# Performance work log

Measured on AMD Instinct MI355X. Metric: run time of the kernel, lower is better.

## Reference

```python
import jax, jax.numpy as jnp
from jax import lax
import numpy as np
import math

B, S, I, H = 64, 512, 1024, 1024


def setup_inputs() -> dict:
    key = jax.random.key(0)
    kx, kw, ku, kb = jax.random.split(key, 4)
    stdv = 1.0 / math.sqrt(H)
    x = jax.random.normal(kx, (B, S, I), dtype=jnp.float32)
    # fused gate weights, order [i, f, g, o] along last axis
    W = jax.random.uniform(kw, (I, 4 * H), minval=-stdv, maxval=stdv, dtype=jnp.float32)
    U = jax.random.uniform(ku, (H, 4 * H), minval=-stdv, maxval=stdv, dtype=jnp.float32)
    b = jax.random.uniform(kb, (4 * H,), minval=-stdv, maxval=stdv, dtype=jnp.float32)
    return {"x": x, "W": W, "U": U, "b": b}


def reference(x, W, U, b):
    bsz, seq, _ = x.shape
    hid = U.shape[0]
    # precompute input projection for all timesteps: one big GEMM
    xW = jnp.einsum("bsi,ig->bsg", x, W) + b  # [B, S, 4H]

    def step(carry, xw_t):
        h, c = carry
        gates = xw_t + h @ U  # [B, 4H]
        i_t, f_t, g_t, o_t = jnp.split(gates, 4, axis=-1)
        i_t = jax.nn.sigmoid(i_t)
        f_t = jax.nn.sigmoid(f_t)
        g_t = jnp.tanh(g_t)
        o_t = jax.nn.sigmoid(o_t)
        c = f_t * c + i_t * g_t
        h = o_t * jnp.tanh(c)
        return (h, c), h

    h0 = jnp.zeros((bsz, hid), dtype=x.dtype)
    c0 = jnp.zeros((bsz, hid), dtype=x.dtype)
    (h_t, c_t), hs = lax.scan(step, (h0, c0), xW.transpose(1, 0, 2))
    hidden_seq = hs.transpose(1, 0, 2)  # [B, S, H]
    return hidden_seq, h_t, c_t
```

## Files before the change

kernel.cpp:

```cpp
#include <hip/hip_runtime.h>

#define BB 64
#define SS 512
#define II 1024
#define HH 1024
#define G4 4096
#define NWG_REC 64

typedef unsigned short u16;
typedef unsigned int u32;
typedef unsigned long long u64;

typedef short s16x8 __attribute__((ext_vector_type(8)));
typedef float f32x4 __attribute__((ext_vector_type(4)));

typedef __attribute__((address_space(1))) const u32 as1_uint_t;
typedef __attribute__((address_space(3))) u32 as3_uint_t;

__device__ __forceinline__ u16 f2bf(float f) {
    u32 x = __float_as_uint(f);
    x += 0x7fffu + ((x >> 16) & 1u);
    return (u16)(x >> 16);
}
__device__ __forceinline__ float bf2f(u16 v) {
    return __uint_as_float(((u32)v) << 16);
}
__device__ __forceinline__ f32x4 mfma16(s16x8 a, s16x8 b, f32x4 c) {
    return __builtin_amdgcn_mfma_f32_16x16x32_bf16(a, b, c, 0, 0, 0);
}
__device__ __forceinline__ float fsigm(float x) { return 1.f / (1.f + __expf(-x)); }
__device__ __forceinline__ float ftanh(float x) {
    float e = __expf(2.f * x);
    return (e - 1.f) / (e + 1.f);
}

#define HL(dst, ptr, OFF) \
    asm volatile("global_load_dwordx4 %0, %1, off offset:%2 sc0 sc1" \
                 : "=v"(dst) : "v"(ptr), "n"(OFF))
#define XL32(dst, ptr) \
    asm volatile("global_load_dword %0, %1, off" : "=v"(dst) : "v"(ptr))
#define XL16(dst, ptr) \
    asm volatile("global_load_ushort %0, %1, off" : "=v"(dst) : "v"(ptr))
#define WAITAV(N, A) \
    asm volatile("s_waitcnt vmcnt(%8)" \
                 : "+v"((A)[0]), "+v"((A)[1]), "+v"((A)[2]), "+v"((A)[3]), \
                   "+v"((A)[4]), "+v"((A)[5]), "+v"((A)[6]), "+v"((A)[7]) \
                 : "n"(N))

__global__ __launch_bounds__(256) void k_convert_x(const float* __restrict__ x,
                                                   u16* __restrict__ xb, int n4) {
    int i = blockIdx.x * 256 + threadIdx.x;
    int stride = gridDim.x * 256;
    const float4* xv = (const float4*)x;
    u64* ov = (u64*)xb;
    for (; i < n4; i += stride) {
        float4 v = xv[i];
        u64 o = (u64)f2bf(v.x) | ((u64)f2bf(v.y) << 16) |
                ((u64)f2bf(v.z) << 32) | ((u64)f2bf(v.w) << 48);
        ov[i] = o;
    }
}

__global__ __launch_bounds__(1024) void k_transpose_bf(const float* __restrict__ A,
                                                       u16* __restrict__ At, int R, int C) {
    __shared__ float tile[32][33];
    int cb = blockIdx.x * 32, rb = blockIdx.y * 32;
    int tx = threadIdx.x, ty = threadIdx.y;
    tile[ty][tx] = A[(size_t)(rb + ty) * C + cb + tx];
    __syncthreads();
    At[(size_t)(cb + ty) * R + rb + tx] = f2bf(tile[tx][ty]);
}

__global__ __launch_bounds__(256) void k_zero(u64* hb, u32* cnt) {
    int i = blockIdx.x * 256 + threadIdx.x;
    int stride = gridDim.x * 256;
    const int n = 2 * BB * HH * 2 / 8;
    for (; i < n; i += stride) hb[i] = 0ull;
    if (blockIdx.x == 0 && threadIdx.x == 0) *cnt = 0u;
}

template <bool XW32>
__global__ __launch_bounds__(256) void k_gemm_xw(const u16* __restrict__ Abf,
                                                 const u16* __restrict__ Bt,
                                                 const float* __restrict__ bias,
                                                 void* __restrict__ xw) {
    __shared__ u16 As[128 * 32];
    __shared__ u16 Bs[128 * 32];
    int bid = blockIdx.x;
    int wid = (bid & 7) * 1024 + (bid >> 3);
    int mt = wid & 255, nt = wid >> 8;
    size_t rb = (size_t)mt * 128;
    int cb = nt * 128;
    int tid = threadIdx.x;
    int w = tid >> 6, l = tid & 63;
    int lr = l >> 4, lc = l & 15;
    int wr = (w >> 1) * 64, wc = (w & 1) * 64;
    f32x4 acc[4][4] = {};
    for (int kb = 0; kb < II; kb += 32) {
        __syncthreads();
#pragma unroll
        for (int q = 0; q < 2; ++q) {
            int bo = q * 4096 + w * 1024 + l * 16;
            int row = bo >> 6;
            int off = (bo & 63) >> 1;
            const u16* srcA = Abf + (rb + row) * II + kb + off;
            __builtin_amdgcn_global_load_lds((as1_uint_t*)srcA,
                (as3_uint_t*)((char*)As + q * 4096 + w * 1024), 16, 0, 0);
            const u16* srcB = Bt + (size_t)(cb + row) * II + kb + off;
            __builtin_amdgcn_global_load_lds((as1_uint_t*)srcB,
                (as3_uint_t*)((char*)Bs + q * 4096 + w * 1024), 16, 0, 0);
        }
        __syncthreads();
        s16x8 af[4], bf[4];
#pragma unroll
        for (int m = 0; m < 4; ++m)
            af[m] = *(const s16x8*)(As + (wr + m * 16 + lc) * 32 + lr * 8);
#pragma unroll
        for (int n = 0; n < 4; ++n)
            bf[n] = *(const s16x8*)(Bs + (wc + n * 16 + lc) * 32 + lr * 8);
#pragma unroll
        for (int m = 0; m < 4; ++m)
#pragma unroll
            for (int n = 0; n < 4; ++n)
                acc[m][n] = mfma16(af[m], bf[n], acc[m][n]);
    }
    float bv[4];
#pragma unroll
    for (int n = 0; n < 4; ++n) bv[n] = bias[cb + wc + n * 16 + lc];
#pragma unroll
    for (int m = 0; m < 4; ++m) {
#pragma unroll
        for (int r = 0; r < 4; ++r) {
            size_t g = rb + wr + m * 16 + lr * 4 + r;
            size_t srow = ((g & 511) << 6) | (g >> 9);
#pragma unroll
            for (int n = 0; n < 4; ++n) {
                float v = acc[m][n][r] + bv[n];
                size_t idx = srow * G4 + cb + wc + n * 16 + lc;
                if (XW32) ((float*)xw)[idx] = v;
                else      ((u16*)xw)[idx] = f2bf(v);
            }
        }
    }
}

template <bool XW32>
__global__ __launch_bounds__(256, 1) void k_lstm3(const u16* __restrict__ Ut,
                                                  const void* __restrict__ xw,
                                                  u16* hb, u32* cnt,
                                                  float* __restrict__ out) {
    __shared__ u16 Us[8192 * 8];
    const int j = blockIdx.x;
    const int tid = threadIdx.x;
    const int w = tid >> 6, l = tid & 63;
    const int lr = l >> 4, lc = l & 15;
    const int rowbase = w * 16;
    const int col = j * 16 + lc;

    for (int i = 0; i < 32; ++i) {
        int ch = tid + (i << 8);
        int lc2 = ch & 15, lr2 = (ch >> 4) & 3, g2 = (ch >> 6) & 3, kk2 = ch >> 8;
        const u16* src = Ut + (size_t)(g2 * HH + j * 16 + lc2) * II + kk2 * 32 + lr2 * 8;
        *(s16x8*)(Us + (size_t)ch * 8) = *(const s16x8*)src;
    }

    float cc[4] = {0.f, 0.f, 0.f, 0.f};
    const size_t xwlane = (size_t)(rowbase + lr * 4) * G4 + col;

    const char* xwp[16];
#pragma unroll
    for (int g = 0; g < 4; ++g)
#pragma unroll
        for (int r = 0; r < 4; ++r) {
            size_t e = (size_t)BB * G4 + xwlane + (size_t)r * G4 + (size_t)g * HH;
            xwp[g * 4 + r] = (const char*)xw + (XW32 ? e * 4 : e * 2);
        }

    float cur[16];
#pragma unroll
    for (int g = 0; g < 4; ++g)
#pragma unroll
        for (int r = 0; r < 4; ++r) {
            size_t e = xwlane + (size_t)r * G4 + (size_t)g * HH;
            cur[g * 4 + r] = XW32 ? ((const float*)xw)[e] : bf2f(((const u16*)xw)[e]);
        }
    __syncthreads();

    for (int t = 0; t < SS; ++t) {
        f32x4 acc[4][4];
#pragma unroll
        for (int g = 0; g < 4; ++g) {
#pragma unroll
            for (int r = 0; r < 4; ++r) acc[g][0][r] = cur[g * 4 + r];
            acc[g][1] = f32x4{0.f, 0.f, 0.f, 0.f};
            acc[g][2] = f32x4{0.f, 0.f, 0.f, 0.f};
            acc[g][3] = f32x4{0.f, 0.f, 0.f, 0.f};
        }

        const u16* hrow = hb + (size_t)(t & 1) * (BB * HH) +
                          (size_t)(rowbase + lc) * HH + lr * 8;
        s16x8 av[32];
#pragma unroll
        for (int kk = 0; kk < 32; ++kk) HL(av[kk], hrow, kk * 64);

        u32 nxt[16];
#pragma unroll
        for (int q = 0; q < 16; ++q) {
            if (XW32) { XL32(nxt[q], xwp[q]); }
            else      { XL16(nxt[q], xwp[q]); }
        }

#pragma unroll
        for (int kb = 0; kb < 4; ++kb) {
            WAITAV(40 - 8 * kb, av + kb * 8);
#pragma unroll
            for (int u = 0; u < 8; ++u) {
                const int kk = kb * 8 + u;
#pragma unroll
                for (int g = 0; g < 4; ++g) {
                    const s16x8 bv = *(const s16x8*)(Us + (size_t)(((kk * 4 + g) * 4 + lr) * 16 + lc) * 8);
                    acc[g][kk & 3] = mfma16(av[kk], bv, acc[g][kk & 3]);
                }
            }
        }

        u16* hwr = hb + (size_t)((t + 1) & 1) * (BB * HH);
        float hval[4];
#pragma unroll
        for (int r = 0; r < 4; ++r) {
            float gi = (acc[0][0][r] + acc[0][1][r]) + (acc[0][2][r] + acc[0][3][r]);
            float gf = (acc[1][0][r] + acc[1][1][r]) + (acc[1][2][r] + acc[1][3][r]);
            float gg = (acc[2][0][r] + acc[2][1][r]) + (acc[2][2][r] + acc[2][3][r]);
            float go = (acc[3][0][r] + acc[3][1][r]) + (acc[3][2][r] + acc[3][3][r]);
            float i_ = fsigm(gi);
            float f_ = fsigm(gf);
            float g_ = ftanh(gg);
            float o_ = fsigm(go);
            cc[r] = f_ * cc[r] + i_ * g_;
            hval[r] = o_ * ftanh(cc[r]);
        }
#pragma unroll
        for (int r = 0; r < 4; ++r) {
            int row = rowbase + lr * 4 + r;
            out[(size_t)row * (SS * HH) + (size_t)t * HH + col] = hval[r];
            if (t < SS - 1) {
                __hip_atomic_store(hwr + (size_t)row * HH + col, f2bf(hval[r]),
                                   __ATOMIC_RELAXED, __HIP_MEMORY_SCOPE_AGENT);
            } else {
                out[(size_t)(BB * SS * HH) + (size_t)row * HH + col] = hval[r];
                out[(size_t)(BB * SS * HH + BB * HH) + (size_t)row * HH + col] = cc[r];
            }
        }

        if (t < SS - 1) {
            asm volatile("s_waitcnt vmcnt(0)"
                         : "+v"(nxt[0]), "+v"(nxt[1]), "+v"(nxt[2]), "+v"(nxt[3]),
                           "+v"(nxt[4]), "+v"(nxt[5]), "+v"(nxt[6]), "+v"(nxt[7]),
                           "+v"(nxt[8]), "+v"(nxt[9]), "+v"(nxt[10]), "+v"(nxt[11]),
                           "+v"(nxt[12]), "+v"(nxt[13]), "+v"(nxt[14]), "+v"(nxt[15]));
            __syncthreads();
            if (tid == 0) {
                u32 target = (u32)(t + 1) * NWG_REC;
                u32 old = __hip_atomic_fetch_add(cnt, 1u, __ATOMIC_RELAXED,
                                                 __HIP_MEMORY_SCOPE_AGENT);
                if (old != target - 1) {
                    while (__hip_atomic_load(cnt, __ATOMIC_RELAXED,
                                             __HIP_MEMORY_SCOPE_AGENT) < target)
                        __builtin_amdgcn_s_sleep(1);
                }
            }
            __syncthreads();
            if (t < SS - 2) {
#pragma unroll
                for (int q = 0; q < 16; ++q)
                    xwp[q] += (size_t)BB * G4 * (XW32 ? 4 : 2);
            }
        }
#pragma unroll
        for (int q = 0; q < 16; ++q)
            cur[q] = XW32 ? __uint_as_float(nxt[q]) : __uint_as_float(nxt[q] << 16);
    }
}

extern "C" void kernel_launch(void* const* d_in, const int* in_sizes, int n_in,
                              void* d_out, int out_size, void* d_ws, size_t ws_size,
                              hipStream_t stream) {
    const float* x = (const float*)d_in[0];
    const float* W = (const float*)d_in[1];
    const float* U = (const float*)d_in[2];
    const float* b = (const float*)d_in[3];
    float* out = (float*)d_out;

    size_t xb_b  = (size_t)BB * SS * II * 2;
    size_t wt_b  = (size_t)G4 * II * 2;
    size_t hb_b  = (size_t)2 * BB * HH * 2;
    size_t xw32_b = (size_t)BB * SS * G4 * 4;
    size_t xw16_b = xw32_b / 2;
    size_t base = xb_b + 2 * wt_b;

    int mode = (base + xw32_b + hb_b + 256 <= ws_size) ? 0 : 1;

    char* p = (char*)d_ws;
    u16* xb = (u16*)p;
    u16* Wt = (u16*)(p + xb_b);
    u16* Ut = (u16*)(p + xb_b + wt_b);
    char* q = p + base;
    void* xw = (void*)q;
    q += (mode == 0) ? xw32_b : xw16_b;
    u16* hb = (u16*)q; q += hb_b;
    u32* cnt = (u32*)q;

    k_convert_x<<<2048, 256, 0, stream>>>(x, xb, BB * SS * II / 4);
    k_transpose_bf<<<dim3(G4 / 32, II / 32), dim3(32, 32), 0, stream>>>(W, Wt, II, G4);
    k_transpose_bf<<<dim3(G4 / 32, II / 32), dim3(32, 32), 0, stream>>>(U, Ut, II, G4);
    k_zero<<<64, 256, 0, stream>>>((u64*)hb, cnt);

    if (mode == 0) {
        k_gemm_xw<true><<<8192, 256, 0, stream>>>(xb, Wt, b, xw);
        k_lstm3<true><<<NWG_REC, 256, 0, stream>>>(Ut, xw, hb, cnt, out);
    } else {
        k_gemm_xw<false><<<8192, 256, 0, stream>>>(xb, Wt, b, xw);
        k_lstm3<false><<<NWG_REC, 256, 0, stream>>>(Ut, xw, hb, cnt, out);
    }
}
```

Measured before the change: 5.687 ms.

## Shard grid barrier counters and add spinning filler workgroups to recurrent kernel

The single global arrival counter is replaced by eight counters on separate cache lines. Each recurrent workgroup atomically increments its group's counter, and the waiter polls all eight with coherent loads. The per-step hidden-sequence output stores are moved between the arrival and the wait so they overlap barrier latency. The grid also grows to 256 workgroups: the extra 192 spin on FMA work until a done flag is set, presumably to keep the GPU's clocks or occupancy up. This adds wasted power and depends on all 256 workgroups being co-resident.

```diff
diff --git a/kernel.cpp b/kernel.cpp
--- a/kernel.cpp
+++ b/kernel.cpp
@@ -6,6 +6,7 @@
 #define HH 1024
 #define G4 4096
 #define NWG_REC 64
+#define NWG_TOT 256
 
 typedef unsigned short u16;
 typedef unsigned int u32;
@@ -39,8 +40,6 @@
                  : "=v"(dst) : "v"(ptr), "n"(OFF))
 #define XL32(dst, ptr) \
     asm volatile("global_load_dword %0, %1, off" : "=v"(dst) : "v"(ptr))
-#define XL16(dst, ptr) \
-    asm volatile("global_load_ushort %0, %1, off" : "=v"(dst) : "v"(ptr))
 #define WAITAV(N, A) \
     asm volatile("s_waitcnt vmcnt(%8)" \
                  : "+v"((A)[0]), "+v"((A)[1]), "+v"((A)[2]), "+v"((A)[3]), \
@@ -71,12 +70,12 @@
     At[(size_t)(cb + ty) * R + rb + tx] = f2bf(tile[tx][ty]);
 }
 
-__global__ __launch_bounds__(256) void k_zero(u64* hb, u32* cnt) {
+__global__ __launch_bounds__(256) void k_zero(u64* hb, u64* cnt) {
     int i = blockIdx.x * 256 + threadIdx.x;
     int stride = gridDim.x * 256;
     const int n = 2 * BB * HH * 2 / 8;
     for (; i < n; i += stride) hb[i] = 0ull;
-    if (blockIdx.x == 0 && threadIdx.x == 0) *cnt = 0u;
+    if (blockIdx.x == 0 && threadIdx.x < 512) cnt[threadIdx.x] = 0ull;
 }
 
 template <bool XW32>
@@ -145,13 +144,30 @@
 }
 
 template <bool XW32>
-__global__ __launch_bounds__(256, 1) void k_lstm3(const u16* __restrict__ Ut,
+__global__ __launch_bounds__(256, 1) void k_lstm4(const u16* __restrict__ Ut,
                                                   const void* __restrict__ xw,
                                                   u16* hb, u32* cnt,
                                                   float* __restrict__ out) {
-    __shared__ u16 Us[8192 * 8];
     const int j = blockIdx.x;
     const int tid = threadIdx.x;
+
+    if (j >= NWG_REC) {
+        const u32* dptr = cnt + 512;
+        float a = 1.0f;
+        while (true) {
+            u32 d;
+            asm volatile("global_load_dword %0, %1, off sc0 sc1\n\t"
+                         "s_waitcnt vmcnt(0)" : "=v"(d) : "v"(dptr));
+            if (d) break;
+#pragma unroll 16
+            for (int i = 0; i < 4096; ++i)
+                asm volatile("v_fmac_f32 %0, %1, %2" : "+v"(a) : "v"(1.0000001f), "v"(a));
+        }
+        asm volatile("" :: "v"(a));
+        return;
+    }
+
+    __shared__ u16 Us[8192 * 8];
     const int w = tid >> 6, l = tid & 63;
     const int lr = l >> 4, lc = l & 15;
     const int rowbase = w * 16;
@@ -184,6 +200,8 @@
             size_t e = xwlane + (size_t)r * G4 + (size_t)g * HH;
             cur[g * 4 + r] = XW32 ? ((const float*)xw)[e] : bf2f(((const u16*)xw)[e]);
         }
+
+    u32* mycnt = cnt + (size_t)(j & 7) * 32;
     __syncthreads();
 
     for (int t = 0; t < SS; ++t) {
@@ -207,7 +225,9 @@
 #pragma unroll
         for (int q = 0; q < 16; ++q) {
             if (XW32) { XL32(nxt[q], xwp[q]); }
-            else      { XL16(nxt[q], xwp[q]); }
+            else {
+                asm volatile("global_load_ushort %0, %1, off" : "=v"(nxt[q]) : "v"(xwp[q]));
+            }
         }
 
 #pragma unroll
@@ -224,7 +244,6 @@
             }
         }
 
-        u16* hwr = hb + (size_t)((t + 1) & 1) * (BB * HH);
         float hval[4];
 #pragma unroll
         for (int r = 0; r < 4; ++r) {
@@ -239,34 +258,52 @@
             cc[r] = f_ * cc[r] + i_ * g_;
             hval[r] = o_ * ftanh(cc[r]);
         }
-#pragma unroll
-        for (int r = 0; r < 4; ++r) {
-            int row = rowbase + lr * 4 + r;
-            out[(size_t)row * (SS * HH) + (size_t)t * HH + col] = hval[r];
-            if (t < SS - 1) {
+
+        if (t < SS - 1) {
+            u16* hwr = hb + (size_t)((t + 1) & 1) * (BB * HH);
+#pragma unroll
+            for (int r = 0; r < 4; ++r) {
+                int row = rowbase + lr * 4 + r;
                 __hip_atomic_store(hwr + (size_t)row * HH + col, f2bf(hval[r]),
                                    __ATOMIC_RELAXED, __HIP_MEMORY_SCOPE_AGENT);
-            } else {
-                out[(size_t)(BB * SS * HH) + (size_t)row * HH + col] = hval[r];
-                out[(size_t)(BB * SS * HH + BB * HH) + (size_t)row * HH + col] = cc[r];
-            }
-        }
-
-        if (t < SS - 1) {
+            }
             asm volatile("s_waitcnt vmcnt(0)"
                          : "+v"(nxt[0]), "+v"(nxt[1]), "+v"(nxt[2]), "+v"(nxt[3]),
                            "+v"(nxt[4]), "+v"(nxt[5]), "+v"(nxt[6]), "+v"(nxt[7]),
                            "+v"(nxt[8]), "+v"(nxt[9]), "+v"(nxt[10]), "+v"(nxt[11]),
-                           "+v"(nxt[12]), "+v"(nxt[13]), "+v"(nxt[14]), "+v"(nxt[15]));
+                           "+v"(nxt[12]), "+v"(nxt[13]), "+v"(nxt[14]), "+v"(nxt[15])
+                         :: "memory");
             __syncthreads();
             if (tid == 0) {
-                u32 target = (u32)(t + 1) * NWG_REC;
-                u32 old = __hip_atomic_fetch_add(cnt, 1u, __ATOMIC_RELAXED,
-                                                 __HIP_MEMORY_SCOPE_AGENT);
-                if (old != target - 1) {
-                    while (__hip_atomic_load(cnt, __ATOMIC_RELAXED,
-                                             __HIP_MEMORY_SCOPE_AGENT) < target)
-                        __builtin_amdgcn_s_sleep(1);
+                u32 one = 1u;
+                asm volatile("global_atomic_add %0, %1, off"
+                             :: "v"(mycnt), "v"(one) : "memory");
+            }
+#pragma unroll
+            for (int r = 0; r < 4; ++r) {
+                int row = rowbase + lr * 4 + r;
+                out[(size_t)row * (SS * HH) + (size_t)t * HH + col] = hval[r];
+            }
+            if (tid == 0) {
+                u32 tgt = (u32)(t + 1) * 8u;
+                while (true) {
+                    u32 c0, c1, c2, c3, c4, c5, c6, c7;
+                    asm volatile(
+                        "global_load_dword %0, %8, off sc0 sc1\n\t"
+                        "global_load_dword %1, %8, off offset:128 sc0 sc1\n\t"
+                        "global_load_dword %2, %8, off offset:256 sc0 sc1\n\t"
+                        "global_load_dword %3, %8, off offset:384 sc0 sc1\n\t"
+                        "global_load_dword %4, %8, off offset:512 sc0 sc1\n\t"
+                        "global_load_dword %5, %8, off offset:640 sc0 sc1\n\t"
+                        "global_load_dword %6, %8, off offset:768 sc0 sc1\n\t"
+                        "global_load_dword %7, %8, off offset:896 sc0 sc1\n\t"
+                        "s_waitcnt vmcnt(0)"
+                        : "=v"(c0), "=v"(c1), "=v"(c2), "=v"(c3),
+                          "=v"(c4), "=v"(c5), "=v"(c6), "=v"(c7)
+                        : "v"(cnt));
+                    if (c0 >= tgt && c1 >= tgt && c2 >= tgt && c3 >= tgt &&
+                        c4 >= tgt && c5 >= tgt && c6 >= tgt && c7 >= tgt) break;
+                    __builtin_amdgcn_s_sleep(1);
                 }
             }
             __syncthreads();
@@ -274,6 +311,18 @@
 #pragma unroll
                 for (int q = 0; q < 16; ++q)
                     xwp[q] += (size_t)BB * G4 * (XW32 ? 4 : 2);
+            }
+        } else {
+#pragma unroll
+            for (int r = 0; r < 4; ++r) {
+                int row = rowbase + lr * 4 + r;
+                out[(size_t)row * (SS * HH) + (size_t)t * HH + col] = hval[r];
+                out[(size_t)(BB * SS * HH) + (size_t)row * HH + col] = hval[r];
+                out[(size_t)(BB * SS * HH + BB * HH) + (size_t)row * HH + col] = cc[r];
+            }
+            if (j == 0 && tid == 0) {
+                __hip_atomic_store(cnt + 512, 1u, __ATOMIC_RELAXED,
+                                   __HIP_MEMORY_SCOPE_AGENT);
             }
         }
 #pragma unroll
@@ -298,7 +347,7 @@
     size_t xw16_b = xw32_b / 2;
     size_t base = xb_b + 2 * wt_b;
 
-    int mode = (base + xw32_b + hb_b + 256 <= ws_size) ? 0 : 1;
+    int mode = (base + xw32_b + hb_b + 4096 <= ws_size) ? 0 : 1;
 
     char* p = (char*)d_ws;
     u16* xb = (u16*)p;
@@ -313,13 +362,13 @@
     k_convert_x<<<2048, 256, 0, stream>>>(x, xb, BB * SS * II / 4);
     k_transpose_bf<<<dim3(G4 / 32, II / 32), dim3(32, 32), 0, stream>>>(W, Wt, II, G4);
     k_transpose_bf<<<dim3(G4 / 32, II / 32), dim3(32, 32), 0, stream>>>(U, Ut, II, G4);
-    k_zero<<<64, 256, 0, stream>>>((u64*)hb, cnt);
+    k_zero<<<64, 256, 0, stream>>>((u64*)hb, (u64*)cnt);
 
     if (mode == 0) {
         k_gemm_xw<true><<<8192, 256, 0, stream>>>(xb, Wt, b, xw);
-        k_lstm3<true><<<NWG_REC, 256, 0, stream>>>(Ut, xw, hb, cnt, out);
+        k_lstm4<true><<<NWG_TOT, 256, 0, stream>>>(Ut, xw, hb, cnt, out);
     } else {
         k_gemm_xw<false><<<8192, 256, 0, stream>>>(xb, Wt, b, xw);
-        k_lstm3<false><<<NWG_REC, 256, 0, stream>>>(Ut, xw, hb, cnt, out);
-    }
-}
+        k_lstm4<false><<<NWG_TOT, 256, 0, stream>>>(Ut, xw, hb, cnt, out);
+    }
+}
```

After: 5.044 ms. 11.3% less time.

## Replace global atomic barrier with per-wave flags and tagged hidden-state words

Applied to the files above, without the earlier changes.

The global counter barrier plus two __syncthreads per timestep is replaced by per-wave publish flags that each wave polls directly. Each stored hidden value carries a timestep tag in its low 16 bits, and consumers verify a checksum of the tags before use, re-loading the chunk if data arrived stale. The hidden-state buffer doubles in size to hold the tags, loads are split into chunks that are checked and unpacked with perm, and the xW prefetch moves to after the MMA loop. A dummy FMA spin replaces s_sleep while polling. The aim is to cut per-step barrier latency, at the cost of extra memory traffic and a fragile checksum-based correctness scheme.

```diff
diff --git a/kernel.cpp b/kernel.cpp
--- a/kernel.cpp
+++ b/kernel.cpp
@@ -13,6 +13,7 @@
 
 typedef short s16x8 __attribute__((ext_vector_type(8)));
 typedef float f32x4 __attribute__((ext_vector_type(4)));
+typedef u32   u32x4 __attribute__((ext_vector_type(4)));
 
 typedef __attribute__((address_space(1))) const u32 as1_uint_t;
 typedef __attribute__((address_space(3))) u32 as3_uint_t;
@@ -39,13 +40,17 @@
                  : "=v"(dst) : "v"(ptr), "n"(OFF))
 #define XL32(dst, ptr) \
     asm volatile("global_load_dword %0, %1, off" : "=v"(dst) : "v"(ptr))
-#define XL16(dst, ptr) \
-    asm volatile("global_load_ushort %0, %1, off" : "=v"(dst) : "v"(ptr))
-#define WAITAV(N, A) \
+#define WAITAV8(N, A) \
     asm volatile("s_waitcnt vmcnt(%8)" \
                  : "+v"((A)[0]), "+v"((A)[1]), "+v"((A)[2]), "+v"((A)[3]), \
                    "+v"((A)[4]), "+v"((A)[5]), "+v"((A)[6]), "+v"((A)[7]) \
                  : "n"(N))
+#define ISSUE_CHUNK(s, cc) do { \
+    HL(av[s][0], hrp, (cc)*512 + 0);   HL(av[s][1], hrp, (cc)*512 + 16);  \
+    HL(av[s][2], hrp, (cc)*512 + 128); HL(av[s][3], hrp, (cc)*512 + 144); \
+    HL(av[s][4], hrp, (cc)*512 + 256); HL(av[s][5], hrp, (cc)*512 + 272); \
+    HL(av[s][6], hrp, (cc)*512 + 384); HL(av[s][7], hrp, (cc)*512 + 400); \
+} while (0)
 
 __global__ __launch_bounds__(256) void k_convert_x(const float* __restrict__ x,
                                                    u16* __restrict__ xb, int n4) {
@@ -71,12 +76,12 @@
     At[(size_t)(cb + ty) * R + rb + tx] = f2bf(tile[tx][ty]);
 }
 
-__global__ __launch_bounds__(256) void k_zero(u64* hb, u32* cnt) {
+__global__ __launch_bounds__(256) void k_zero(u64* hb, u64* cnt) {
     int i = blockIdx.x * 256 + threadIdx.x;
     int stride = gridDim.x * 256;
-    const int n = 2 * BB * HH * 2 / 8;
+    const int n = 2 * BB * HH * 4 / 8;
     for (; i < n; i += stride) hb[i] = 0ull;
-    if (blockIdx.x == 0 && threadIdx.x == 0) *cnt = 0u;
+    if (blockIdx.x == 0 && threadIdx.x < 512) cnt[threadIdx.x] = 0ull;
 }
 
 template <bool XW32>
@@ -145,9 +150,9 @@
 }
 
 template <bool XW32>
-__global__ __launch_bounds__(256, 1) void k_lstm3(const u16* __restrict__ Ut,
+__global__ __launch_bounds__(256, 1) void k_lstm5(const u16* __restrict__ Ut,
                                                   const void* __restrict__ xw,
-                                                  u16* hb, u32* cnt,
+                                                  u32* hb32, u32* sync,
                                                   float* __restrict__ out) {
     __shared__ u16 Us[8192 * 8];
     const int j = blockIdx.x;
@@ -184,9 +189,39 @@
             size_t e = xwlane + (size_t)r * G4 + (size_t)g * HH;
             cur[g * 4 + r] = XW32 ? ((const float*)xw)[e] : bf2f(((const u16*)xw)[e]);
         }
+
+    const u32* cpoll = sync + w * 64 + l;
+    u32* cpub = sync + w * 64 + j;
+    float burn = 1.0f;
+    const float burnc = 1.0000001f;
+
     __syncthreads();
 
     for (int t = 0; t < SS; ++t) {
+        {
+            u32 cv;
+            while (true) {
+                asm volatile("global_load_dword %0, %1, off sc0 sc1\n\t"
+                             "s_waitcnt vmcnt(0)"
+                             : "=v"(cv) : "v"(cpoll) : "memory");
+                if (__all((int)(cv >= (u32)t))) break;
+#pragma unroll
+                for (int i = 0; i < 16; ++i)
+                    asm volatile("v_fmac_f32 %0, %1, %2" : "+v"(burn) : "v"(burnc), "v"(burn));
+            }
+        }
+
+        u32 nxt[16];
+        if (t > 0) {
+            asm volatile("" : "+v"(nxt[0]), "+v"(nxt[1]), "+v"(nxt[2]), "+v"(nxt[3]),
+                             "+v"(nxt[4]), "+v"(nxt[5]), "+v"(nxt[6]), "+v"(nxt[7]),
+                             "+v"(nxt[8]), "+v"(nxt[9]), "+v"(nxt[10]), "+v"(nxt[11]),
+                             "+v"(nxt[12]), "+v"(nxt[13]), "+v"(nxt[14]), "+v"(nxt[15]));
+#pragma unroll
+            for (int q = 0; q < 16; ++q)
+                cur[q] = XW32 ? __uint_as_float(nxt[q]) : __uint_as_float(nxt[q] << 16);
+        }
+
         f32x4 acc[4][4];
 #pragma unroll
         for (int g = 0; g < 4; ++g) {
@@ -197,34 +232,69 @@
             acc[g][3] = f32x4{0.f, 0.f, 0.f, 0.f};
         }
 
-        const u16* hrow = hb + (size_t)(t & 1) * (BB * HH) +
-                          (size_t)(rowbase + lc) * HH + lr * 8;
-        s16x8 av[32];
-#pragma unroll
-        for (int kk = 0; kk < 32; ++kk) HL(av[kk], hrow, kk * 64);
-
-        u32 nxt[16];
-#pragma unroll
-        for (int q = 0; q < 16; ++q) {
-            if (XW32) { XL32(nxt[q], xwp[q]); }
-            else      { XL16(nxt[q], xwp[q]); }
-        }
-
-#pragma unroll
-        for (int kb = 0; kb < 4; ++kb) {
-            WAITAV(40 - 8 * kb, av + kb * 8);
-#pragma unroll
-            for (int u = 0; u < 8; ++u) {
-                const int kk = kb * 8 + u;
+        const u32* hrp = hb32 + ((size_t)(t & 1) << 16) +
+                         (size_t)(rowbase + lc) * 1024 + lr * 8;
+        u32x4 av[4][8];
+        ISSUE_CHUNK(0, 0); ISSUE_CHUNK(1, 1); ISSUE_CHUNK(2, 2); ISSUE_CHUNK(3, 3);
+
+        constexpr int WT[8] = {24, 24, 24, 24, 24, 16, 8, 0};
+        const u32 expsum = 32u * (u32)t;
+#pragma unroll
+        for (int c = 0; c < 8; ++c) {
+            const int s = c & 3;
+            WAITAV8(WT[c], av[s]);
+            u32x4 t0 = av[s][0] + av[s][1], t1 = av[s][2] + av[s][3];
+            u32x4 t2 = av[s][4] + av[s][5], t3 = av[s][6] + av[s][7];
+            u32x4 t4 = t0 + t1 + t2 + t3;
+            u32 sum = t4.x + t4.y + t4.z + t4.w;
+            while (__any((int)(((sum - expsum) & 0xFFFFu) != 0u))) {
+                ISSUE_CHUNK(s, c);
+                WAITAV8(0, av[s]);
+                u32x4 r0 = av[s][0] + av[s][1], r1 = av[s][2] + av[s][3];
+                u32x4 r2 = av[s][4] + av[s][5], r3 = av[s][6] + av[s][7];
+                u32x4 r4 = r0 + r1 + r2 + r3;
+                sum = r4.x + r4.y + r4.z + r4.w;
+            }
+            s16x8 pk[4];
+#pragma unroll
+            for (int kq = 0; kq < 4; ++kq) {
+                u32x4 xlo = av[s][2 * kq], xhi = av[s][2 * kq + 1];
+                union { u32 u[4]; s16x8 v; } p;
+                p.u[0] = __builtin_amdgcn_perm(xlo.y, xlo.x, 0x07060302);
+                p.u[1] = __builtin_amdgcn_perm(xlo.w, xlo.z, 0x07060302);
+                p.u[2] = __builtin_amdgcn_perm(xhi.y, xhi.x, 0x07060302);
+                p.u[3] = __builtin_amdgcn_perm(xhi.w, xhi.z, 0x07060302);
+                pk[kq] = p.v;
+            }
+            if (c < 4) ISSUE_CHUNK(s, c + 4);
+#pragma unroll
+            for (int kq = 0; kq < 4; ++kq) {
+                const int kk = c * 4 + kq;
 #pragma unroll
                 for (int g = 0; g < 4; ++g) {
-                    const s16x8 bv = *(const s16x8*)(Us + (size_t)(((kk * 4 + g) * 4 + lr) * 16 + lc) * 8);
-                    acc[g][kk & 3] = mfma16(av[kk], bv, acc[g][kk & 3]);
+                    const s16x8 bv = *(const s16x8*)(Us +
+                        (size_t)(((kk * 4 + g) * 4 + lr) * 16 + lc) * 8);
+                    acc[g][kq] = mfma16(pk[kq], bv, acc[g][kq]);
                 }
             }
         }
 
-        u16* hwr = hb + (size_t)((t + 1) & 1) * (BB * HH);
+        if (t < SS - 1) {
+#pragma unroll
+            for (int q = 0; q < 16; ++q) {
+                if (XW32) { XL32(nxt[q], xwp[q]); }
+                else {
+                    asm volatile("global_load_ushort %0, %1, off"
+                                 : "=v"(nxt[q]) : "v"(xwp[q]));
+                }
+            }
+            if (t < SS - 2) {
+#pragma unroll
+                for (int q = 0; q < 16; ++q)
+                    xwp[q] += (size_t)BB * G4 * (XW32 ? 4 : 2);
+            }
+        }
+
         float hval[4];
 #pragma unroll
         for (int r = 0; r < 4; ++r) {
@@ -239,47 +309,37 @@
             cc[r] = f_ * cc[r] + i_ * g_;
             hval[r] = o_ * ftanh(cc[r]);
         }
-#pragma unroll
-        for (int r = 0; r < 4; ++r) {
-            int row = rowbase + lr * 4 + r;
-            out[(size_t)row * (SS * HH) + (size_t)t * HH + col] = hval[r];
-            if (t < SS - 1) {
-                __hip_atomic_store(hwr + (size_t)row * HH + col, f2bf(hval[r]),
-                                   __ATOMIC_RELAXED, __HIP_MEMORY_SCOPE_AGENT);
-            } else {
+
+        if (t < SS - 1) {
+            u32* hwp = hb32 + ((size_t)((t + 1) & 1) << 16);
+            const u32 tagv = (u32)(t + 1);
+#pragma unroll
+            for (int r = 0; r < 4; ++r) {
+                int row = rowbase + lr * 4 + r;
+                u32 val = ((u32)f2bf(hval[r]) << 16) | tagv;
+                u32* ad = hwp + (size_t)row * 1024 + col;
+                asm volatile("global_store_dword %0, %1, off sc0 sc1"
+                             :: "v"(ad), "v"(val) : "memory");
+            }
+            if (l == 0)
+                asm volatile("global_store_dword %0, %1, off sc0 sc1"
+                             :: "v"(cpub), "v"(tagv) : "memory");
+#pragma unroll
+            for (int r = 0; r < 4; ++r) {
+                int row = rowbase + lr * 4 + r;
+                out[(size_t)row * (SS * HH) + (size_t)t * HH + col] = hval[r];
+            }
+        } else {
+#pragma unroll
+            for (int r = 0; r < 4; ++r) {
+                int row = rowbase + lr * 4 + r;
+                out[(size_t)row * (SS * HH) + (size_t)t * HH + col] = hval[r];
                 out[(size_t)(BB * SS * HH) + (size_t)row * HH + col] = hval[r];
                 out[(size_t)(BB * SS * HH + BB * HH) + (size_t)row * HH + col] = cc[r];
             }
         }
-
-        if (t < SS - 1) {
-            asm volatile("s_waitcnt vmcnt(0)"
-                         : "+v"(nxt[0]), "+v"(nxt[1]), "+v"(nxt[2]), "+v"(nxt[3]),
-                           "+v"(nxt[4]), "+v"(nxt[5]), "+v"(nxt[6]), "+v"(nxt[7]),
-                           "+v"(nxt[8]), "+v"(nxt[9]), "+v"(nxt[10]), "+v"(nxt[11]),
-                           "+v"(nxt[12]), "+v"(nxt[13]), "+v"(nxt[14]), "+v"(nxt[15]));
-            __syncthreads();
-            if (tid == 0) {
-                u32 target = (u32)(t + 1) * NWG_REC;
-                u32 old = __hip_atomic_fetch_add(cnt, 1u, __ATOMIC_RELAXED,
-                                                 __HIP_MEMORY_SCOPE_AGENT);
-                if (old != target - 1) {
-                    while (__hip_atomic_load(cnt, __ATOMIC_RELAXED,
-                                             __HIP_MEMORY_SCOPE_AGENT) < target)
-                        __builtin_amdgcn_s_sleep(1);
-                }
-            }
-            __syncthreads();
-            if (t < SS - 2) {
-#pragma unroll
-                for (int q = 0; q < 16; ++q)
-                    xwp[q] += (size_t)BB * G4 * (XW32 ? 4 : 2);
-            }
-        }
-#pragma unroll
-        for (int q = 0; q < 16; ++q)
-            cur[q] = XW32 ? __uint_as_float(nxt[q]) : __uint_as_float(nxt[q] << 16);
-    }
+    }
+    asm volatile("" :: "v"(burn));
 }
 
 extern "C" void kernel_launch(void* const* d_in, const int* in_sizes, int n_in,
@@ -293,12 +353,12 @@
 
     size_t xb_b  = (size_t)BB * SS * II * 2;
     size_t wt_b  = (size_t)G4 * II * 2;
-    size_t hb_b  = (size_t)2 * BB * HH * 2;
+    size_t hb_b  = (size_t)2 * BB * HH * 4;
     size_t xw32_b = (size_t)BB * SS * G4 * 4;
     size_t xw16_b = xw32_b / 2;
     size_t base = xb_b + 2 * wt_b;
 
-    int mode = (base + xw32_b + hb_b + 256 <= ws_size) ? 0 : 1;
+    int mode = (base + xw32_b + hb_b + 4096 <= ws_size) ? 0 : 1;
 
     char* p = (char*)d_ws;
     u16* xb = (u16*)p;
@@ -307,19 +367,19 @@
     char* q = p + base;
     void* xw = (void*)q;
     q += (mode == 0) ? xw32_b : xw16_b;
-    u16* hb = (u16*)q; q += hb_b;
-    u32* cnt = (u32*)q;
+    u32* hb32 = (u32*)q; q += hb_b;
+    u32* sync = (u32*)q;
 
     k_convert_x<<<2048, 256, 0, stream>>>(x, xb, BB * SS * II / 4);
     k_transpose_bf<<<dim3(G4 / 32, II / 32), dim3(32, 32), 0, stream>>>(W, Wt, II, G4);
     k_transpose_bf<<<dim3(G4 / 32, II / 32), dim3(32, 32), 0, stream>>>(U, Ut, II, G4);
-    k_zero<<<64, 256, 0, stream>>>((u64*)hb, cnt);
+    k_zero<<<64, 256, 0, stream>>>((u64*)hb32, (u64*)sync);
 
     if (mode == 0) {
         k_gemm_xw<true><<<8192, 256, 0, stream>>>(xb, Wt, b, xw);
-        k_lstm3<true><<<NWG_REC, 256, 0, stream>>>(Ut, xw, hb, cnt, out);
+        k_lstm5<true><<<NWG_REC, 256, 0, stream>>>(Ut, xw, hb32, sync, out);
     } else {
         k_gemm_xw<false><<<8192, 256, 0, stream>>>(xb, Wt, b, xw);
-        k_lstm3<false><<<NWG_REC, 256, 0, stream>>>(Ut, xw, hb, cnt, out);
-    }
-}
+        k_lstm5<false><<<NWG_REC, 256, 0, stream>>>(Ut, xw, hb32, sync, out);
+    }
+}
```

Measured after the change: 6.189 ms. 8.8% more time.
